# Performance work log

Hardware: AMD Instinct MI355X
Metric: run time of the kernel (lower is better)

Reference implementation:

```python
import jax, jax.numpy as jnp
import numpy as np

EMBED_DIM = 1024
NUM_HEADS = 16
HEAD_DIM = EMBED_DIM // NUM_HEADS
B, S = 4, 1024


def setup_inputs() -> dict:
    key = jax.random.key(0)
    kq, kk, kw, kb, kd = jax.random.split(key, 5)
    q = jax.random.normal(kq, (B, NUM_HEADS, S, HEAD_DIM), dtype=jnp.float32)
    k = jax.random.normal(kk, (B, NUM_HEADS, S, HEAD_DIM), dtype=jnp.float32)
    # nn.Bilinear(out_features=1) weight per head is [1, D, D]; stacked -> [H, D, D]
    W = jax.random.normal(kw, (NUM_HEADS, HEAD_DIM, HEAD_DIM), dtype=jnp.float32) * (1.0 / np.sqrt(HEAD_DIM))
    b = jax.random.normal(kb, (NUM_HEADS,), dtype=jnp.float32) * 0.02
    Wd = jnp.full((NUM_HEADS,), 0.5, dtype=jnp.float32)  # init tt.tensor(0.5)
    return {"q": q, "k": k, "W": W, "b": b, "Wd": Wd}


def reference(q, k, W, b, Wd):
    scale = EMBED_DIM ** 0.5
    # raw scaled logits: note original multiplies by sqrt(embed_dim)
    d = jnp.einsum("bhid,bhjd->bhij", q, k) * scale
    # per-pair bilinear score: q_i^T W_h k_j + b_h, gated by Wd_h
    bil = jnp.einsum("bhid,hde,bhje->bhij", q, W, k)
    d = d + (bil + b[None, :, None, None]) * Wd[None, :, None, None]
    return d
```

## Files before the change

### kernel.cpp

```cpp
#include <hip/hip_runtime.h>

#define S_LEN 1024
#define HD 64
#define NBH 64

typedef __attribute__((ext_vector_type(8))) short short8;
typedef __attribute__((ext_vector_type(4))) float floatx4;
typedef __attribute__((ext_vector_type(4))) unsigned short ushort4v;

__device__ __forceinline__ unsigned short f2bf(float f) {
  unsigned int u = __builtin_bit_cast(unsigned int, f);
  u += 0x7fffu + ((u >> 16) & 1u);
  return (unsigned short)(u >> 16);
}

__global__ __launch_bounds__(256) void prep_small_kernel(
    const float* __restrict__ W, const float* __restrict__ Wd,
    unsigned short* __restrict__ MT) {
  int idx = blockIdx.x * 256 + threadIdx.x;
  int h  = idx >> 12;
  int n  = (idx >> 6) & 63;
  int kk = idx & 63;
  float v = Wd[h] * W[(h << 12) + (kk << 6) + n];
  if (kk == n) v += 32.0f;
  MT[idx] = f2bf(v);
}

__global__ __launch_bounds__(256) void convert_k_kernel(
    const float* __restrict__ k, unsigned short* __restrict__ kp) {
  size_t t = (size_t)blockIdx.x * 256 + threadIdx.x;
  floatx4 v = *(const floatx4*)(k + t * 4);
  ushort4v o;
  o[0] = f2bf(v[0]); o[1] = f2bf(v[1]); o[2] = f2bf(v[2]); o[3] = f2bf(v[3]);
  *(ushort4v*)(kp + t * 4) = o;
}

__global__ __launch_bounds__(256) void prep_q_kernel(
    const float* __restrict__ q, const unsigned short* __restrict__ MT,
    unsigned short* __restrict__ qp) {
  const int bh   = blockIdx.y;
  const int h    = bh & 15;
  const int wave = threadIdx.x >> 6;
  const int lane = threadIdx.x & 63;
  const int l15  = lane & 15;
  const int quad = lane >> 4;
  const int i0   = blockIdx.x * 64 + wave * 16;

  const float* __restrict__ qb = q + (size_t)bh * S_LEN * HD;
  const unsigned short* __restrict__ mt = MT + (h << 12);

  short8 bfrag[4][2];
#pragma unroll
  for (int nt = 0; nt < 4; nt++)
#pragma unroll
    for (int ks = 0; ks < 2; ks++)
      bfrag[nt][ks] = *(const short8*)(mt + (nt * 16 + l15) * HD + ks * 32 + quad * 8);

  short8 afrag[2];
#pragma unroll
  for (int ks = 0; ks < 2; ks++) {
    const float* src = qb + (size_t)(i0 + l15) * HD + ks * 32 + quad * 8;
    floatx4 a0 = *(const floatx4*)src;
    floatx4 a1 = *(const floatx4*)(src + 4);
    short8 f;
    f[0] = f2bf(a0[0]); f[1] = f2bf(a0[1]); f[2] = f2bf(a0[2]); f[3] = f2bf(a0[3]);
    f[4] = f2bf(a1[0]); f[5] = f2bf(a1[1]); f[6] = f2bf(a1[2]); f[7] = f2bf(a1[3]);
    afrag[ks] = f;
  }

  floatx4 acc[4];
#pragma unroll
  for (int nt = 0; nt < 4; nt++) {
    acc[nt] = (floatx4){0.f, 0.f, 0.f, 0.f};
#pragma unroll
    for (int ks = 0; ks < 2; ks++)
      acc[nt] = __builtin_amdgcn_mfma_f32_16x16x32_bf16(afrag[ks], bfrag[nt][ks],
                                                        acc[nt], 0, 0, 0);
  }

  unsigned short* __restrict__ qpb = qp + (size_t)bh * S_LEN * HD;
#pragma unroll
  for (int nt = 0; nt < 4; nt++)
#pragma unroll
    for (int r = 0; r < 4; r++)
      qpb[(i0 + quad * 4 + r) * HD + nt * 16 + l15] = f2bf(acc[nt][r]);
}

#define LPAD 68
__global__ __launch_bounds__(256) void main_kernel(
    const unsigned short* __restrict__ qp, const unsigned short* __restrict__ kp,
    const float* __restrict__ b, const float* __restrict__ Wd,
    float* __restrict__ out) {
  __shared__ __align__(16) float lds[4 * 32 * LPAD];

  const int bh   = blockIdx.z;
  const int h    = bh & 15;
  const int wave = threadIdx.x >> 6;
  const int lane = threadIdx.x & 63;
  const int l15  = lane & 15;
  const int quad = lane >> 4;
  const int row0 = blockIdx.y * 128 + (wave >> 1) * 64;
  const int col0 = blockIdx.x * 128 + (wave & 1) * 64;

  const unsigned short* __restrict__ qb = qp + ((size_t)bh << 16);
  const unsigned short* __restrict__ kb = kp + ((size_t)bh << 16);

  short8 afrag[4][2], bfrag[4][2];
#pragma unroll
  for (int t = 0; t < 4; t++)
#pragma unroll
    for (int ks = 0; ks < 2; ks++) {
      afrag[t][ks] = *(const short8*)(qb + (row0 + t * 16 + l15) * HD + ks * 32 + quad * 8);
      bfrag[t][ks] = *(const short8*)(kb + (col0 + t * 16 + l15) * HD + ks * 32 + quad * 8);
    }

  const float cbias = Wd[h] * b[h];
  floatx4 acc[4][4];
#pragma unroll
  for (int mtile = 0; mtile < 4; mtile++)
#pragma unroll
    for (int nt = 0; nt < 4; nt++) {
      acc[mtile][nt] = (floatx4){cbias, cbias, cbias, cbias};
#pragma unroll
      for (int ks = 0; ks < 2; ks++)
        acc[mtile][nt] = __builtin_amdgcn_mfma_f32_16x16x32_bf16(
            afrag[mtile][ks], bfrag[nt][ks], acc[mtile][nt], 0, 0, 0);
    }

  float* __restrict__ wlds = lds + wave * (32 * LPAD);
  float* __restrict__ ob = out + ((size_t)bh << 20);
#pragma unroll
  for (int c = 0; c < 2; ++c) {
#pragma unroll
    for (int mr = 0; mr < 2; ++mr) {
      int mtile = 2 * c + mr;
#pragma unroll
      for (int nt = 0; nt < 4; nt++)
#pragma unroll
        for (int r = 0; r < 4; r++)
          wlds[(mr * 16 + quad * 4 + r) * LPAD + nt * 16 + l15] = acc[mtile][nt][r];
    }
    __asm__ volatile("s_waitcnt lgkmcnt(0)" ::: "memory");
#pragma unroll
    for (int g = 0; g < 8; ++g) {
      int row = g * 4 + quad;
      floatx4 v = *(const floatx4*)(wlds + row * LPAD + l15 * 4);
      __builtin_nontemporal_store(
          v, (floatx4*)(ob + (size_t)(row0 + c * 32 + row) * S_LEN + col0 + l15 * 4));
    }
    __asm__ volatile("s_waitcnt lgkmcnt(0)" ::: "memory");
  }
}

extern "C" void kernel_launch(void* const* d_in, const int* in_sizes, int n_in,
                              void* d_out, int out_size, void* d_ws, size_t ws_size,
                              hipStream_t stream) {
  const float* q  = (const float*)d_in[0];
  const float* k  = (const float*)d_in[1];
  const float* W  = (const float*)d_in[2];
  const float* b  = (const float*)d_in[3];
  const float* Wd = (const float*)d_in[4];
  float* out = (float*)d_out;

  unsigned short* qp = (unsigned short*)d_ws;
  unsigned short* kp = qp + (size_t)NBH * S_LEN * HD;
  unsigned short* MT = kp + (size_t)NBH * S_LEN * HD;

  prep_small_kernel<<<256, 256, 0, stream>>>(W, Wd, MT);
  convert_k_kernel<<<4096, 256, 0, stream>>>(k, kp);
  prep_q_kernel<<<dim3(16, NBH), 256, 0, stream>>>(q, MT, qp);
  main_kernel<<<dim3(8, 8, NBH), 256, 0, stream>>>(qp, kp, b, Wd, out);
}
```

Measured before the change: 306.3 us.

## Fuse k conversion and q-projection into main kernel via LDS staging

Removes the separate convert_k and prep_q kernels. Each main-kernel block now loads its 128-row q and k tiles from fp32, converts them to bf16, computes the q·M projection with MFMA, and stages both in shared memory before the main MFMA tile. This removes two launches and the bf16 intermediate write/read round trip. The cost is redundant work: every block recomputes the projection and conversion for its tiles, eight times over across the grid, with fp32 reads from L2. The output stores also switch from nontemporal to normal stores.

```diff
diff --git a/kernel.cpp b/kernel.cpp
--- a/kernel.cpp
+++ b/kernel.cpp
@@ -6,12 +6,18 @@
 
 typedef __attribute__((ext_vector_type(8))) short short8;
 typedef __attribute__((ext_vector_type(4))) float floatx4;
-typedef __attribute__((ext_vector_type(4))) unsigned short ushort4v;
 
 __device__ __forceinline__ unsigned short f2bf(float f) {
   unsigned int u = __builtin_bit_cast(unsigned int, f);
   u += 0x7fffu + ((u >> 16) & 1u);
   return (unsigned short)(u >> 16);
+}
+
+__device__ __forceinline__ short8 cvt8(floatx4 a0, floatx4 a1) {
+  short8 f;
+  f[0] = f2bf(a0[0]); f[1] = f2bf(a0[1]); f[2] = f2bf(a0[2]); f[3] = f2bf(a0[3]);
+  f[4] = f2bf(a1[0]); f[5] = f2bf(a1[1]); f[6] = f2bf(a1[2]); f[7] = f2bf(a1[3]);
+  return f;
 }
 
 __global__ __launch_bounds__(256) void prep_small_kernel(
@@ -26,72 +32,17 @@
   MT[idx] = f2bf(v);
 }
 
-__global__ __launch_bounds__(256) void convert_k_kernel(
-    const float* __restrict__ k, unsigned short* __restrict__ kp) {
-  size_t t = (size_t)blockIdx.x * 256 + threadIdx.x;
-  floatx4 v = *(const floatx4*)(k + t * 4);
-  ushort4v o;
-  o[0] = f2bf(v[0]); o[1] = f2bf(v[1]); o[2] = f2bf(v[2]); o[3] = f2bf(v[3]);
-  *(ushort4v*)(kp + t * 4) = o;
-}
+#define QROW 72
+#define LPAD 68
 
-__global__ __launch_bounds__(256) void prep_q_kernel(
-    const float* __restrict__ q, const unsigned short* __restrict__ MT,
-    unsigned short* __restrict__ qp) {
-  const int bh   = blockIdx.y;
-  const int h    = bh & 15;
-  const int wave = threadIdx.x >> 6;
-  const int lane = threadIdx.x & 63;
-  const int l15  = lane & 15;
-  const int quad = lane >> 4;
-  const int i0   = blockIdx.x * 64 + wave * 16;
-
-  const float* __restrict__ qb = q + (size_t)bh * S_LEN * HD;
-  const unsigned short* __restrict__ mt = MT + (h << 12);
-
-  short8 bfrag[4][2];
-#pragma unroll
-  for (int nt = 0; nt < 4; nt++)
-#pragma unroll
-    for (int ks = 0; ks < 2; ks++)
-      bfrag[nt][ks] = *(const short8*)(mt + (nt * 16 + l15) * HD + ks * 32 + quad * 8);
-
-  short8 afrag[2];
-#pragma unroll
-  for (int ks = 0; ks < 2; ks++) {
-    const float* src = qb + (size_t)(i0 + l15) * HD + ks * 32 + quad * 8;
-    floatx4 a0 = *(const floatx4*)src;
-    floatx4 a1 = *(const floatx4*)(src + 4);
-    short8 f;
-    f[0] = f2bf(a0[0]); f[1] = f2bf(a0[1]); f[2] = f2bf(a0[2]); f[3] = f2bf(a0[3]);
-    f[4] = f2bf(a1[0]); f[5] = f2bf(a1[1]); f[6] = f2bf(a1[2]); f[7] = f2bf(a1[3]);
-    afrag[ks] = f;
-  }
-
-  floatx4 acc[4];
-#pragma unroll
-  for (int nt = 0; nt < 4; nt++) {
-    acc[nt] = (floatx4){0.f, 0.f, 0.f, 0.f};
-#pragma unroll
-    for (int ks = 0; ks < 2; ks++)
-      acc[nt] = __builtin_amdgcn_mfma_f32_16x16x32_bf16(afrag[ks], bfrag[nt][ks],
-                                                        acc[nt], 0, 0, 0);
-  }
-
-  unsigned short* __restrict__ qpb = qp + (size_t)bh * S_LEN * HD;
-#pragma unroll
-  for (int nt = 0; nt < 4; nt++)
-#pragma unroll
-    for (int r = 0; r < 4; r++)
-      qpb[(i0 + quad * 4 + r) * HD + nt * 16 + l15] = f2bf(acc[nt][r]);
-}
-
-#define LPAD 68
-__global__ __launch_bounds__(256) void main_kernel(
-    const unsigned short* __restrict__ qp, const unsigned short* __restrict__ kp,
+__global__ __launch_bounds__(256) void fused_kernel(
+    const float* __restrict__ q, const float* __restrict__ k,
+    const unsigned short* __restrict__ MT,
     const float* __restrict__ b, const float* __restrict__ Wd,
     float* __restrict__ out) {
-  __shared__ __align__(16) float lds[4 * 32 * LPAD];
+  __shared__ __align__(16) unsigned short smem[2 * 128 * QROW];
+  unsigned short* __restrict__ qlds = smem;
+  unsigned short* __restrict__ klds = smem + 128 * QROW;
 
   const int bh   = blockIdx.z;
   const int h    = bh & 15;
@@ -99,20 +50,75 @@
   const int lane = threadIdx.x & 63;
   const int l15  = lane & 15;
   const int quad = lane >> 4;
-  const int row0 = blockIdx.y * 128 + (wave >> 1) * 64;
-  const int col0 = blockIdx.x * 128 + (wave & 1) * 64;
 
-  const unsigned short* __restrict__ qb = qp + ((size_t)bh << 16);
-  const unsigned short* __restrict__ kb = kp + ((size_t)bh << 16);
+  const float* __restrict__ qg = q + ((size_t)bh << 16);
+  const float* __restrict__ kg = k + ((size_t)bh << 16);
+  const unsigned short* __restrict__ mt = MT + (h << 12);
 
+  {
+    const int rbase = wave * 32 + (lane >> 3);
+    const int col   = (lane & 7) * 8;
+#pragma unroll
+    for (int it = 0; it < 4; ++it) {
+      int rl = rbase + it * 8;
+      const float* src = kg + (size_t)(blockIdx.x * 128 + rl) * HD + col;
+      floatx4 a0 = *(const floatx4*)src;
+      floatx4 a1 = *(const floatx4*)(src + 4);
+      *(short8*)(klds + rl * QROW + col) = cvt8(a0, a1);
+    }
+  }
+
+  {
+    short8 bm[4][2];
+#pragma unroll
+    for (int nt = 0; nt < 4; nt++)
+#pragma unroll
+      for (int ks = 0; ks < 2; ks++)
+        bm[nt][ks] = *(const short8*)(mt + (nt * 16 + l15) * HD + ks * 32 + quad * 8);
+
+    short8 aq[2][2];
+#pragma unroll
+    for (int m = 0; m < 2; m++)
+#pragma unroll
+      for (int ks = 0; ks < 2; ks++) {
+        const float* src = qg + (size_t)(blockIdx.y * 128 + wave * 32 + m * 16 + l15) * HD
+                              + ks * 32 + quad * 8;
+        aq[m][ks] = cvt8(*(const floatx4*)src, *(const floatx4*)(src + 4));
+      }
+
+    floatx4 accq[2][4];
+#pragma unroll
+    for (int m = 0; m < 2; m++)
+#pragma unroll
+      for (int nt = 0; nt < 4; nt++) {
+        accq[m][nt] = (floatx4){0.f, 0.f, 0.f, 0.f};
+#pragma unroll
+        for (int ks = 0; ks < 2; ks++)
+          accq[m][nt] = __builtin_amdgcn_mfma_f32_16x16x32_bf16(
+              aq[m][ks], bm[nt][ks], accq[m][nt], 0, 0, 0);
+      }
+#pragma unroll
+    for (int m = 0; m < 2; m++)
+#pragma unroll
+      for (int nt = 0; nt < 4; nt++)
+#pragma unroll
+        for (int r = 0; r < 4; r++)
+          qlds[(wave * 32 + m * 16 + quad * 4 + r) * QROW + nt * 16 + l15] =
+              f2bf(accq[m][nt][r]);
+  }
+  __syncthreads();
+
+  const int wr0 = (wave >> 1) * 64;
+  const int wc0 = (wave & 1) * 64;
   short8 afrag[4][2], bfrag[4][2];
 #pragma unroll
   for (int t = 0; t < 4; t++)
 #pragma unroll
     for (int ks = 0; ks < 2; ks++) {
-      afrag[t][ks] = *(const short8*)(qb + (row0 + t * 16 + l15) * HD + ks * 32 + quad * 8);
-      bfrag[t][ks] = *(const short8*)(kb + (col0 + t * 16 + l15) * HD + ks * 32 + quad * 8);
+      afrag[t][ks] = *(const short8*)(qlds + (wr0 + t * 16 + l15) * QROW + ks * 32 + quad * 8);
+      bfrag[t][ks] = *(const short8*)(klds + (wc0 + t * 16 + l15) * QROW + ks * 32 + quad * 8);
     }
+  __syncthreads();
 
   const float cbias = Wd[h] * b[h];
   floatx4 acc[4][4];
@@ -127,7 +133,10 @@
             afrag[mtile][ks], bfrag[nt][ks], acc[mtile][nt], 0, 0, 0);
     }
 
-  float* __restrict__ wlds = lds + wave * (32 * LPAD);
+  const int row0 = blockIdx.y * 128 + wr0;
+  const int col0 = blockIdx.x * 128 + wc0;
+  float* __restrict__ elds = (float*)(void*)smem;
+  float* __restrict__ wlds = elds + wave * (32 * LPAD);
   float* __restrict__ ob = out + ((size_t)bh << 20);
 #pragma unroll
   for (int c = 0; c < 2; ++c) {
@@ -145,8 +154,7 @@
     for (int g = 0; g < 8; ++g) {
       int row = g * 4 + quad;
       floatx4 v = *(const floatx4*)(wlds + row * LPAD + l15 * 4);
-      __builtin_nontemporal_store(
-          v, (floatx4*)(ob + (size_t)(row0 + c * 32 + row) * S_LEN + col0 + l15 * 4));
+      *(floatx4*)(ob + (size_t)(row0 + c * 32 + row) * S_LEN + col0 + l15 * 4) = v;
     }
     __asm__ volatile("s_waitcnt lgkmcnt(0)" ::: "memory");
   }
@@ -162,12 +170,8 @@
   const float* Wd = (const float*)d_in[4];
   float* out = (float*)d_out;
 
-  unsigned short* qp = (unsigned short*)d_ws;
-  unsigned short* kp = qp + (size_t)NBH * S_LEN * HD;
-  unsigned short* MT = kp + (size_t)NBH * S_LEN * HD;
+  unsigned short* MT = (unsigned short*)d_ws;
 
   prep_small_kernel<<<256, 256, 0, stream>>>(W, Wd, MT);
-  convert_k_kernel<<<4096, 256, 0, stream>>>(k, kp);
-  prep_q_kernel<<<dim3(16, NBH), 256, 0, stream>>>(q, MT, qp);
-  main_kernel<<<dim3(8, 8, NBH), 256, 0, stream>>>(qp, kp, b, Wd, out);
+  fused_kernel<<<dim3(8, 8, NBH), 256, 0, stream>>>(q, k, MT, b, Wd, out);
 }
```

Result: slower. 320.2 us (+4.5%).

## Loop each main-kernel block over four column tiles with double-buffered K fragments

Applied to the files above, without the earlier changes.

Each block of the main kernel now keeps its Q fragments in registers and walks four 128-column tiles of K, prefetching the next tile's K fragments while computing and storing the current one. The grid shrinks fourfold in the column dimension. The aim is to reuse Q loads, amortize per-block setup, and overlap K loads with MFMA and output stores. In exchange there are fewer blocks to spread across CUs and higher register pressure from the doubled B fragments, which may lower occupancy.

```diff
diff --git a/kernel.cpp b/kernel.cpp
--- a/kernel.cpp
+++ b/kernel.cpp
@@ -99,56 +99,78 @@
   const int lane = threadIdx.x & 63;
   const int l15  = lane & 15;
   const int quad = lane >> 4;
-  const int row0 = blockIdx.y * 128 + (wave >> 1) * 64;
-  const int col0 = blockIdx.x * 128 + (wave & 1) * 64;
+  const int row0 = blockIdx.x * 128 + (wave >> 1) * 64;
+  const int colw = (wave & 1) * 64;
+  const int colbase = blockIdx.y * 512;
 
   const unsigned short* __restrict__ qb = qp + ((size_t)bh << 16);
   const unsigned short* __restrict__ kb = kp + ((size_t)bh << 16);
 
-  short8 afrag[4][2], bfrag[4][2];
+  short8 afrag[4][2];
 #pragma unroll
   for (int t = 0; t < 4; t++)
 #pragma unroll
-    for (int ks = 0; ks < 2; ks++) {
+    for (int ks = 0; ks < 2; ks++)
       afrag[t][ks] = *(const short8*)(qb + (row0 + t * 16 + l15) * HD + ks * 32 + quad * 8);
-      bfrag[t][ks] = *(const short8*)(kb + (col0 + t * 16 + l15) * HD + ks * 32 + quad * 8);
+
+  const float cbias = Wd[h] * b[h];
+  float* __restrict__ wlds = lds + wave * (32 * LPAD);
+  float* __restrict__ ob = out + ((size_t)bh << 20);
+
+  short8 bfrag[2][4][2];
+#pragma unroll
+  for (int t = 0; t < 4; t++)
+#pragma unroll
+    for (int ks = 0; ks < 2; ks++)
+      bfrag[0][t][ks] =
+          *(const short8*)(kb + (colbase + colw + t * 16 + l15) * HD + ks * 32 + quad * 8);
+
+#pragma unroll
+  for (int c = 0; c < 4; ++c) {
+    if (c < 3) {
+      const int coln = colbase + (c + 1) * 128 + colw;
+#pragma unroll
+      for (int t = 0; t < 4; t++)
+#pragma unroll
+        for (int ks = 0; ks < 2; ks++)
+          bfrag[(c + 1) & 1][t][ks] =
+              *(const short8*)(kb + (coln + t * 16 + l15) * HD + ks * 32 + quad * 8);
     }
 
-  const float cbias = Wd[h] * b[h];
-  floatx4 acc[4][4];
+    floatx4 acc[4][4];
 #pragma unroll
-  for (int mtile = 0; mtile < 4; mtile++)
+    for (int mt = 0; mt < 4; mt++)
 #pragma unroll
-    for (int nt = 0; nt < 4; nt++) {
-      acc[mtile][nt] = (floatx4){cbias, cbias, cbias, cbias};
+      for (int nt = 0; nt < 4; nt++) {
+        acc[mt][nt] = (floatx4){cbias, cbias, cbias, cbias};
 #pragma unroll
-      for (int ks = 0; ks < 2; ks++)
-        acc[mtile][nt] = __builtin_amdgcn_mfma_f32_16x16x32_bf16(
-            afrag[mtile][ks], bfrag[nt][ks], acc[mtile][nt], 0, 0, 0);
+        for (int ks = 0; ks < 2; ks++)
+          acc[mt][nt] = __builtin_amdgcn_mfma_f32_16x16x32_bf16(
+              afrag[mt][ks], bfrag[c & 1][nt][ks], acc[mt][nt], 0, 0, 0);
+      }
+
+    const int col0 = colbase + c * 128 + colw;
+#pragma unroll
+    for (int ch = 0; ch < 2; ++ch) {
+#pragma unroll
+      for (int mr = 0; mr < 2; ++mr) {
+        int mtile = 2 * ch + mr;
+#pragma unroll
+        for (int nt = 0; nt < 4; nt++)
+#pragma unroll
+          for (int r = 0; r < 4; r++)
+            wlds[(mr * 16 + quad * 4 + r) * LPAD + nt * 16 + l15] = acc[mtile][nt][r];
+      }
+      __asm__ volatile("s_waitcnt lgkmcnt(0)" ::: "memory");
+#pragma unroll
+      for (int g = 0; g < 8; ++g) {
+        int row = g * 4 + quad;
+        floatx4 v = *(const floatx4*)(wlds + row * LPAD + l15 * 4);
+        __builtin_nontemporal_store(
+            v, (floatx4*)(ob + (size_t)(row0 + ch * 32 + row) * S_LEN + col0 + l15 * 4));
+      }
+      __asm__ volatile("s_waitcnt lgkmcnt(0)" ::: "memory");
     }
-
-  float* __restrict__ wlds = lds + wave * (32 * LPAD);
-  float* __restrict__ ob = out + ((size_t)bh << 20);
-#pragma unroll
-  for (int c = 0; c < 2; ++c) {
-#pragma unroll
-    for (int mr = 0; mr < 2; ++mr) {
-      int mtile = 2 * c + mr;
-#pragma unroll
-      for (int nt = 0; nt < 4; nt++)
-#pragma unroll
-        for (int r = 0; r < 4; r++)
-          wlds[(mr * 16 + quad * 4 + r) * LPAD + nt * 16 + l15] = acc[mtile][nt][r];
-    }
-    __asm__ volatile("s_waitcnt lgkmcnt(0)" ::: "memory");
-#pragma unroll
-    for (int g = 0; g < 8; ++g) {
-      int row = g * 4 + quad;
-      floatx4 v = *(const floatx4*)(wlds + row * LPAD + l15 * 4);
-      __builtin_nontemporal_store(
-          v, (floatx4*)(ob + (size_t)(row0 + c * 32 + row) * S_LEN + col0 + l15 * 4));
-    }
-    __asm__ volatile("s_waitcnt lgkmcnt(0)" ::: "memory");
   }
 }
 
@@ -169,5 +191,5 @@
   prep_small_kernel<<<256, 256, 0, stream>>>(W, Wd, MT);
   convert_k_kernel<<<4096, 256, 0, stream>>>(k, kp);
   prep_q_kernel<<<dim3(16, NBH), 256, 0, stream>>>(q, MT, qp);
-  main_kernel<<<dim3(8, 8, NBH), 256, 0, stream>>>(qp, kp, b, Wd, out);
+  main_kernel<<<dim3(8, 2, NBH), 256, 0, stream>>>(qp, kp, b, Wd, out);
 }
```

New measurement: 310.9 us. No clear change (+1.5%).
